# Performance work log

Measured on AMD Instinct MI355X. Metric: run time of the kernel, lower is better.

Reference implementation:

```python
import jax, jax.numpy as jnp
import numpy as np

B, N, E, K = 4, 8192, 1024, 2048  # batch, points, emb_dims, pool nodes (N//4)
KNN = 20


def _conv(w, x):  # 1x1 Conv1d, no bias: w [O,C], x [B,C,N]
    return jnp.einsum('oc,bcn->bon', w, x)


def _bn(x, s, b):  # eval-mode BN folded to per-channel scale/bias, x [B,C,N]
    return x * s[None, :, None] + b[None, :, None]


def _sqdist(a, b):  # a [B,3,N], b [B,3,M] -> [B,N,M] squared distances
    return ((a * a).sum(1)[:, :, None] + (b * b).sum(1)[:, None, :]
            - 2.0 * jnp.einsum('bcn,bcm->bnm', a, b))


def _bgather(f, idx):  # f [B,C,N], idx [B,...] -> [B,C,...]
    return jax.vmap(lambda ff, ii: ff[:, ii])(f, idx)


def _pool(xyz, feat, pw, pb, k):
    Bq, C, _ = feat.shape
    proj = _conv(pw, feat) + pb[None, :, None]          # [B,8C,N]
    vec = proj.max(-1).reshape(Bq, C, 8)                # [B,C,8]
    scores = jax.nn.sigmoid(jnp.einsum('bcn,bce->bne', feat, vec))  # [B,N,8]
    v, i = jax.lax.top_k(scores.transpose(0, 2, 1), k // 8)         # [B,8,k//8]
    values = v.transpose(0, 2, 1).reshape(Bq, -1)       # [B,k] (torch reshape order)
    idx = i.transpose(0, 2, 1).reshape(Bq, -1)
    node_static = _bgather(xyz, idx)                    # [B,3,k]
    node_feature = _bgather(feat, idx) * values[:, None, :]
    node = node_static * values[:, None, :]
    return node, node_feature, node_static


def _aggregate(xyz, node, feat, k):
    d = _sqdist(xyz, node)                               # [B,N,M]
    _, idx = jax.lax.top_k(-d.transpose(0, 2, 1), k)     # [B,M,k] nearest inputs per node
    grouped = _bgather(feat, idx)                        # [B,C,M,k]
    return grouped.max(-1)                               # [B,C,M]


def _unpool(node_xyz, unknown_xyz, feat):
    d = _sqdist(unknown_xyz, node_xyz)                   # [B,N,M]
    negd, idx = jax.lax.top_k(-d, 3)                     # 3-NN along M
    w = jax.nn.softmax(-negd, axis=-1)                   # softmax over sq-dists (faithful)
    grouped = _bgather(feat, idx)                        # [B,C,N,3]
    return (w[:, None, :, :] * grouped).sum(-1)


def _forward(x, conv1_w, bn1_s, bn1_b, conv2_w, bn2_s, bn2_b,
             conv2m_w, bn2m_s, bn2m_b, pool_w, pool_b,
             conv3_w, bn3_s, bn3_b, conv4_w, bn4_s, bn4_b,
             conv5_w, bn5_s, bn5_b, conv6_w, bn6c_s, bn6c_b,
             conv7_w, bn7c_s, bn7c_b, conv8_w, bn8_s, bn8_b,
             conv9_w, bn9_s, bn9_b, conv10_w,
             lin1_w, bn6h_s, bn6h_b, lin2_w, lin2_b, bn7h_s, bn7h_b,
             lin3_w, lin3_b):
    relu = jax.nn.relu
    xyz = x
    x1 = relu(_bn(_conv(conv1_w, x), bn1_s, bn1_b))      # [B,64,N]
    x2 = relu(_bn(_conv(conv2_w, x1), bn2_s, bn2_b))     # [B,64,N]
    xt1_ = jnp.concatenate([x1, x2], 1)                  # [B,128,N]
    xt1 = relu(_bn(_conv(conv2m_w, xt1_), bn2m_s, bn2m_b))  # [B,E,N]
    node1, nf1, node1_static = _pool(xyz, xt1_, pool_w, pool_b, K)
    agg = _aggregate(xyz, node1, xt1_, KNN)              # [B,128,K]
    h = jnp.concatenate([nf1, agg], 1)                   # [B,256,K]
    x3 = relu(_bn(_conv(conv3_w, h), bn3_s, bn3_b))
    x4 = relu(_bn(_conv(conv4_w, x3), bn4_s, bn4_b))
    xt2 = relu(_bn(_conv(conv5_w, jnp.concatenate([x3, x4], 1)), bn5_s, bn5_b))
    vector = jnp.concatenate([xt1.max(-1), xt2.max(-1)], 1)  # [B,2E]
    c = relu((vector @ lin1_w.T) * bn6h_s + bn6h_b)
    c = relu((c @ lin2_w.T + lin2_b) * bn7h_s + bn7h_b)
    logits_cls = c @ lin3_w.T + lin3_b                   # [B,15]
    vrep = jnp.broadcast_to(vector[:, :, None], (vector.shape[0], vector.shape[1], x4.shape[-1]))
    s = relu(_bn(_conv(conv6_w, jnp.concatenate([vrep, x4], 1)), bn6c_s, bn6c_b))
    s = relu(_bn(_conv(conv7_w, jnp.concatenate([s, x3], 1)), bn7c_s, bn7c_b))
    s = _unpool(node1, xyz, s)                           # [B,128,N]
    s = relu(_bn(_conv(conv8_w, jnp.concatenate([s, x2], 1)), bn8_s, bn8_b))
    s = relu(_bn(_conv(conv9_w, jnp.concatenate([s, x1], 1)), bn9_s, bn9_b))
    logits_seg = _conv(conv10_w, s)                      # [B,2,N]
    return (logits_cls, logits_seg, node1, node1_static)


def setup_inputs() -> dict:
    key = jax.random.key(0)
    keys = iter(jax.random.split(key, 80))
    def w(shape, scale=0.05):
        return jax.random.normal(next(keys), shape, jnp.float32) * scale
    inp = {'x': jax.random.normal(next(keys), (B, 3, N), jnp.float32)}
    conv_shapes = {'conv1_w': (64, 3), 'conv2_w': (64, 64), 'conv2m_w': (E, 128),
                   'conv3_w': (256, 256), 'conv4_w': (256, 256), 'conv5_w': (E, 512),
                   'conv6_w': (128, 2 * E + 256), 'conv7_w': (128, 384),
                   'conv8_w': (128, 192), 'conv9_w': (128, 192), 'conv10_w': (2, 128)}
    for n, s in conv_shapes.items():
        inp[n] = w(s)
    for n, c in [('bn1', 64), ('bn2', 64), ('bn2m', E), ('bn3', 256), ('bn4', 256),
                 ('bn5', E), ('bn6c', 128), ('bn7c', 128), ('bn8', 128), ('bn9', 128),
                 ('bn6h', 512), ('bn7h', 256)]:
        inp[n + '_s'] = 1.0 + w((c,))
        inp[n + '_b'] = w((c,))
    inp['pool_w'] = w((E, 128)); inp['pool_b'] = w((E,))
    inp['lin1_w'] = w((512, 2 * E))
    inp['lin2_w'] = w((256, 512)); inp['lin2_b'] = w((256,))
    inp['lin3_w'] = w((15, 256)); inp['lin3_b'] = w((15,))
    return inp


def reference(x, conv1_w, bn1_s, bn1_b, conv2_w, bn2_s, bn2_b,
              conv2m_w, bn2m_s, bn2m_b, pool_w, pool_b,
              conv3_w, bn3_s, bn3_b, conv4_w, bn4_s, bn4_b,
              conv5_w, bn5_s, bn5_b, conv6_w, bn6c_s, bn6c_b,
              conv7_w, bn7c_s, bn7c_b, conv8_w, bn8_s, bn8_b,
              conv9_w, bn9_s, bn9_b, conv10_w,
              lin1_w, bn6h_s, bn6h_b, lin2_w, lin2_b, bn7h_s, bn7h_b,
              lin3_w, lin3_b):
    return _forward(x, conv1_w, bn1_s, bn1_b, conv2_w, bn2_s, bn2_b,
                    conv2m_w, bn2m_s, bn2m_b, pool_w, pool_b,
                    conv3_w, bn3_s, bn3_b, conv4_w, bn4_s, bn4_b,
                    conv5_w, bn5_s, bn5_b, conv6_w, bn6c_s, bn6c_b,
                    conv7_w, bn7c_s, bn7c_b, conv8_w, bn8_s, bn8_b,
                    conv9_w, bn9_s, bn9_b, conv10_w,
                    lin1_w, bn6h_s, bn6h_b, lin2_w, lin2_b, bn7h_s, bn7h_b,
                    lin3_w, lin3_b)
```

## Files before the change

### kernel.cpp

```cpp
#include <hip/hip_runtime.h>
#include <math.h>

#define NPTS 8192
#define MNODE 2048

#define WS_XT1  0L
#define WS_A    4194304L
#define WS_B    8388608L
#define WS_C    12582912L
#define WS_D    14680064L
#define WS_TOPV 18874368L
#define WS_TOPI 18882560L
#define WS_NODE 18890752L
#define WS_MAXP 18915328L
#define WS_VEC  18919424L
#define WS_C1   18927616L
#define WS_C2   18929664L
#define WS_B6   18930688L
#define WS_K20  18931200L
#define WS_K3I  19095040L
#define WS_K3W  19193344L

__global__ __launch_bounds__(256) void k_conv1(const float* __restrict__ x,
                                               const float* __restrict__ W,
                                               const float* __restrict__ sc,
                                               const float* __restrict__ bi,
                                               float* __restrict__ out) {
    int t = blockIdx.x * 256 + threadIdx.x;
    int n = t & 8191, o = (t >> 13) & 63, b = t >> 19;
    const float* xb = x + (long)b * 3 * NPTS;
    float a = W[o * 3 + 0] * xb[n] + W[o * 3 + 1] * xb[NPTS + n] + W[o * 3 + 2] * xb[2 * NPTS + n];
    a = fmaxf(a * sc[o] + bi[o], 0.f);
    out[((long)b * 128 + o) * NPTS + n] = a;
}

__global__ __launch_bounds__(256) void k_conv2(const float* __restrict__ in,
                                               const float* __restrict__ W,
                                               const float* __restrict__ sc,
                                               const float* __restrict__ bi,
                                               float* __restrict__ out) {
    int t = blockIdx.x * 256 + threadIdx.x;
    int n = t & 8191, o = (t >> 13) & 63, b = t >> 19;
    const float* ip = in + (long)b * 128 * NPTS + n;
    const float* wp = W + o * 64;
    float a = 0.f;
#pragma unroll 8
    for (int c = 0; c < 64; ++c) a = fmaf(wp[c], ip[(long)c * NPTS], a);
    out[((long)b * 128 + 64 + o) * NPTS + n] = fmaxf(a * sc[o] + bi[o], 0.f);
}

#define CMAX_FMA16()                                                        \
    {                                                                       \
        const float4* wp4 = reinterpret_cast<const float4*>(Wl + c16);      \
        _Pragma("unroll")                                                   \
        for (int g = 0; g < 4; ++g) {                                       \
            float4 w = wp4[g];                                              \
            acc[4 * g + 0].x = fmaf(w.x, v.x, acc[4 * g + 0].x);            \
            acc[4 * g + 0].y = fmaf(w.x, v.y, acc[4 * g + 0].y);            \
            acc[4 * g + 0].z = fmaf(w.x, v.z, acc[4 * g + 0].z);            \
            acc[4 * g + 0].w = fmaf(w.x, v.w, acc[4 * g + 0].w);            \
            acc[4 * g + 1].x = fmaf(w.y, v.x, acc[4 * g + 1].x);            \
            acc[4 * g + 1].y = fmaf(w.y, v.y, acc[4 * g + 1].y);            \
            acc[4 * g + 1].z = fmaf(w.y, v.z, acc[4 * g + 1].z);            \
            acc[4 * g + 1].w = fmaf(w.y, v.w, acc[4 * g + 1].w);            \
            acc[4 * g + 2].x = fmaf(w.z, v.x, acc[4 * g + 2].x);            \
            acc[4 * g + 2].y = fmaf(w.z, v.y, acc[4 * g + 2].y);            \
            acc[4 * g + 2].z = fmaf(w.z, v.z, acc[4 * g + 2].z);            \
            acc[4 * g + 2].w = fmaf(w.z, v.w, acc[4 * g + 2].w);            \
            acc[4 * g + 3].x = fmaf(w.w, v.x, acc[4 * g + 3].x);            \
            acc[4 * g + 3].y = fmaf(w.w, v.y, acc[4 * g + 3].y);            \
            acc[4 * g + 3].z = fmaf(w.w, v.z, acc[4 * g + 3].z);            \
            acc[4 * g + 3].w = fmaf(w.w, v.w, acc[4 * g + 3].w);            \
        }                                                                   \
    }

__global__ __launch_bounds__(256) void k_convmax(
        const float* __restrict__ in, int C, long ibs,
        const float* __restrict__ W1, const float* __restrict__ cb1,
        const float* __restrict__ sc1, const float* __restrict__ bi1, int relu1,
        float* __restrict__ pmax1,
        const float* __restrict__ W2, const float* __restrict__ cb2,
        const float* __restrict__ sc2, const float* __restrict__ bi2, int relu2,
        float* __restrict__ pmax2,
        int wpitch, int O, int Nn) {
    extern __shared__ float sm_[];
    float* Wl = sm_;
    float* red = sm_ + 16 * C;
    int b = blockIdx.z;
    int ns = blockIdx.x;
    int oblocks = O >> 4;
    int setid = (int)blockIdx.y / oblocks;
    int og0 = ((int)blockIdx.y - setid * oblocks) * 16;
    const float* W  = setid ? W2 : W1;
    const float* cb = setid ? cb2 : cb1;
    const float* sc = setid ? sc2 : sc1;
    const float* bi = setid ? bi2 : bi1;
    int do_relu     = setid ? relu2 : relu1;
    float* pmax     = setid ? pmax2 : pmax1;
    for (int t = threadIdx.x; t < 16 * C; t += 256) {
        int c = t >> 4, o = t & 15;
        Wl[t] = W[(long)(og0 + o) * wpitch + c];
    }
    __syncthreads();
    int n0 = ns * 1024 + threadIdx.x * 4;
    float4 acc[16];
#pragma unroll
    for (int o = 0; o < 16; ++o) acc[o] = make_float4(0.f, 0.f, 0.f, 0.f);
    const float* p = in + (long)b * ibs + n0;
    float4 v = *reinterpret_cast<const float4*>(p);
    for (int c = 0; c < C - 1; ++c) {
        float4 vn = *reinterpret_cast<const float4*>(p + (long)(c + 1) * Nn);
        int c16 = c * 16;
        CMAX_FMA16();
        v = vn;
    }
    {
        int c16 = (C - 1) * 16;
        CMAX_FMA16();
    }
#pragma unroll
    for (int o = 0; o < 16; ++o) {
        float cbv = cb ? cb[og0 + o] : 0.f;
        float scv = sc ? sc[og0 + o] : 1.f;
        float biv = bi ? bi[og0 + o] : 0.f;
        float4 a = acc[o];
        float vx = (a.x + cbv) * scv + biv;
        float vy = (a.y + cbv) * scv + biv;
        float vz = (a.z + cbv) * scv + biv;
        float vw = (a.w + cbv) * scv + biv;
        if (do_relu) {
            vx = fmaxf(vx, 0.f); vy = fmaxf(vy, 0.f);
            vz = fmaxf(vz, 0.f); vw = fmaxf(vw, 0.f);
        }
        red[o * 257 + threadIdx.x] = fmaxf(fmaxf(vx, vy), fmaxf(vz, vw));
    }
    __syncthreads();
    for (int ls = 7; ls >= 0; --ls) {
        int s = 1 << ls;
        for (int w = threadIdx.x; w < 16 * s; w += 256) {
            int o = w >> ls, i = w & (s - 1);
            float* r = red + o * 257;
            r[i] = fmaxf(r[i], r[i + s]);
        }
        __syncthreads();
    }
    if (threadIdx.x < 16)
        pmax[((long)ns * 4 + b) * O + og0 + threadIdx.x] = red[threadIdx.x * 257];
}

__global__ __launch_bounds__(256) void k_maxred(const float* __restrict__ pmax, int nsplit,
                                                int O, float* __restrict__ out, long obs) {
    int t = blockIdx.x * 256 + threadIdx.x;
    if (t >= 4 * O) return;
    int o = t % O, b = t / O;
    float m = -3.0e38f;
    for (int s = 0; s < nsplit; ++s) m = fmaxf(m, pmax[((long)s * 4 + b) * O + o]);
    out[(long)b * obs + o] = m;
}

#define CONV_FMA8()                                                         \
    {                                                                       \
        const float4* wp4 = reinterpret_cast<const float4*>(Wl + c8);       \
        _Pragma("unroll")                                                   \
        for (int g = 0; g < 2; ++g) {                                       \
            float4 w = wp4[g];                                              \
            acc[4 * g + 0].x = fmaf(w.x, v.x, acc[4 * g + 0].x);            \
            acc[4 * g + 0].y = fmaf(w.x, v.y, acc[4 * g + 0].y);            \
            acc[4 * g + 0].z = fmaf(w.x, v.z, acc[4 * g + 0].z);            \
            acc[4 * g + 0].w = fmaf(w.x, v.w, acc[4 * g + 0].w);            \
            acc[4 * g + 1].x = fmaf(w.y, v.x, acc[4 * g + 1].x);            \
            acc[4 * g + 1].y = fmaf(w.y, v.y, acc[4 * g + 1].y);            \
            acc[4 * g + 1].z = fmaf(w.y, v.z, acc[4 * g + 1].z);            \
            acc[4 * g + 1].w = fmaf(w.y, v.w, acc[4 * g + 1].w);            \
            acc[4 * g + 2].x = fmaf(w.z, v.x, acc[4 * g + 2].x);            \
            acc[4 * g + 2].y = fmaf(w.z, v.y, acc[4 * g + 2].y);            \
            acc[4 * g + 2].z = fmaf(w.z, v.z, acc[4 * g + 2].z);            \
            acc[4 * g + 2].w = fmaf(w.z, v.w, acc[4 * g + 2].w);            \
            acc[4 * g + 3].x = fmaf(w.w, v.x, acc[4 * g + 3].x);            \
            acc[4 * g + 3].y = fmaf(w.w, v.y, acc[4 * g + 3].y);            \
            acc[4 * g + 3].z = fmaf(w.w, v.z, acc[4 * g + 3].z);            \
            acc[4 * g + 3].w = fmaf(w.w, v.w, acc[4 * g + 3].w);            \
        }                                                                   \
    }

__global__ __launch_bounds__(256) void k_conv(const float* __restrict__ in1, int C1, long ibs1,
                                              const float* __restrict__ in2, int C2, long ibs2,
                                              const float* __restrict__ W, int wpitch,
                                              const float* __restrict__ extra,
                                              const float* __restrict__ sc,
                                              const float* __restrict__ bi, int do_relu,
                                              float* __restrict__ out, long obs, int O, int Nn) {
    __shared__ float Wl[384 * 8];
    int b = blockIdx.z;
    int og0 = blockIdx.y * 8;
    int on = O - og0; if (on > 8) on = 8;
    int Ct = C1 + C2;
    for (int t = threadIdx.x; t < Ct * 8; t += 256) {
        int c = t >> 3, o = t & 7;
        Wl[t] = (o < on) ? W[(long)(og0 + o) * wpitch + c] : 0.f;
    }
    __syncthreads();
    int n0 = blockIdx.x * 1024 + threadIdx.x * 4;
    float4 acc[8];
#pragma unroll
    for (int o = 0; o < 8; ++o) acc[o] = make_float4(0.f, 0.f, 0.f, 0.f);
    const float* p1 = in1 + (long)b * ibs1 + n0;
    {
        float4 v = *reinterpret_cast<const float4*>(p1);
        for (int c = 0; c < C1 - 1; ++c) {
            float4 vn = *reinterpret_cast<const float4*>(p1 + (long)(c + 1) * Nn);
            int c8 = c * 8;
            CONV_FMA8();
            v = vn;
        }
        int c8 = (C1 - 1) * 8;
        CONV_FMA8();
    }
    if (in2) {
        const float* p2 = in2 + (long)b * ibs2 + n0;
        float4 v = *reinterpret_cast<const float4*>(p2);
        for (int c = 0; c < C2 - 1; ++c) {
            float4 vn = *reinterpret_cast<const float4*>(p2 + (long)(c + 1) * Nn);
            int c8 = (C1 + c) * 8;
            CONV_FMA8();
            v = vn;
        }
        int c8 = (Ct - 1) * 8;
        CONV_FMA8();
    }
#pragma unroll
    for (int o = 0; o < 8; ++o) {
        if (o < on) {
            float e = extra ? extra[(long)b * O + og0 + o] : 0.f;
            float s = sc ? sc[og0 + o] : 1.f;
            float bv = bi ? bi[og0 + o] : 0.f;
            float4 a = acc[o];
            a.x = (a.x + e) * s + bv;
            a.y = (a.y + e) * s + bv;
            a.z = (a.z + e) * s + bv;
            a.w = (a.w + e) * s + bv;
            if (do_relu) {
                a.x = fmaxf(a.x, 0.f); a.y = fmaxf(a.y, 0.f);
                a.z = fmaxf(a.z, 0.f); a.w = fmaxf(a.w, 0.f);
            }
            *reinterpret_cast<float4*>(out + (long)b * obs + (long)(og0 + o) * Nn + n0) = a;
        }
    }
}

__global__ __launch_bounds__(256) void k_scores(const float* __restrict__ feat,
                                                const float* __restrict__ maxp,
                                                float* __restrict__ scores) {
    __shared__ float vl[1024];
    int b = blockIdx.z;
    for (int t = threadIdx.x; t < 1024; t += 256) vl[t] = maxp[b * 1024 + t];
    __syncthreads();
    int n0 = blockIdx.x * 1024 + threadIdx.x * 4;
    float4 acc[8];
#pragma unroll
    for (int e = 0; e < 8; ++e) acc[e] = make_float4(0.f, 0.f, 0.f, 0.f);
    const float* p = feat + (long)b * 128 * NPTS + n0;
    for (int c = 0; c < 128; ++c) {
        float4 v = *reinterpret_cast<const float4*>(p + (long)c * NPTS);
#pragma unroll
        for (int e = 0; e < 8; ++e) {
            float w = vl[c * 8 + e];
            acc[e].x = fmaf(w, v.x, acc[e].x);
            acc[e].y = fmaf(w, v.y, acc[e].y);
            acc[e].z = fmaf(w, v.z, acc[e].z);
            acc[e].w = fmaf(w, v.w, acc[e].w);
        }
    }
#pragma unroll
    for (int e = 0; e < 8; ++e) {
        float4 a = acc[e];
        a.x = 1.f / (1.f + expf(-a.x));
        a.y = 1.f / (1.f + expf(-a.y));
        a.z = 1.f / (1.f + expf(-a.z));
        a.w = 1.f / (1.f + expf(-a.w));
        *reinterpret_cast<float4*>(scores + ((long)b * 8 + e) * NPTS + n0) = a;
    }
}

__global__ __launch_bounds__(256) void k_sorta(const float* __restrict__ scores,
                                               unsigned int* __restrict__ kout,
                                               unsigned short* __restrict__ iout) {
    __shared__ unsigned int kv[1024];
    __shared__ unsigned short ki[1024];
    int ch = blockIdx.x & 7;
    const float* sp = scores + (long)(blockIdx.x >> 3) * NPTS + ch * 1024;
    for (int t = threadIdx.x; t < 1024; t += 256) {
        kv[t] = __float_as_uint(sp[t]) ^ 0xFFFFFFFFu;
        ki[t] = (unsigned short)(ch * 1024 + t);
    }
    __syncthreads();
    for (int k = 2; k <= 1024; k <<= 1) {
        for (int j = k >> 1; j > 0; j >>= 1) {
            for (int t = threadIdx.x; t < 1024; t += 256) {
                int ixj = t ^ j;
                if (ixj > t) {
                    unsigned int va = kv[t], vb = kv[ixj];
                    unsigned short ia = ki[t], ib = ki[ixj];
                    bool up = ((t & k) == 0);
                    bool gt = (va > vb) || (va == vb && ia > ib);
                    if (gt == up) { kv[t] = vb; kv[ixj] = va; ki[t] = ib; ki[ixj] = ia; }
                }
            }
            __syncthreads();
        }
    }
    if (threadIdx.x < 256) {
        kout[blockIdx.x * 256 + threadIdx.x] = kv[threadIdx.x];
        iout[blockIdx.x * 256 + threadIdx.x] = ki[threadIdx.x];
    }
}

__global__ __launch_bounds__(512) void k_sortb(const unsigned int* __restrict__ kin,
                                               const unsigned short* __restrict__ iin,
                                               float* __restrict__ topv,
                                               int* __restrict__ topi) {
    __shared__ unsigned int kv[2048];
    __shared__ unsigned short ki[2048];
    int be = blockIdx.x, b = be >> 3, e = be & 7;
    for (int t = threadIdx.x; t < 2048; t += 512) {
        kv[t] = kin[be * 2048 + t];
        ki[t] = iin[be * 2048 + t];
    }
    __syncthreads();
    for (int k = 2; k <= 2048; k <<= 1) {
        for (int j = k >> 1; j > 0; j >>= 1) {
            for (int t = threadIdx.x; t < 2048; t += 512) {
                int ixj = t ^ j;
                if (ixj > t) {
                    unsigned int va = kv[t], vb = kv[ixj];
                    unsigned short ia = ki[t], ib = ki[ixj];
                    bool up = ((t & k) == 0);
                    bool gt = (va > vb) || (va == vb && ia > ib);
                    if (gt == up) { kv[t] = vb; kv[ixj] = va; ki[t] = ib; ki[ixj] = ia; }
                }
            }
            __syncthreads();
        }
    }
    for (int r = threadIdx.x; r < 256; r += 512) {
        int j = r * 8 + e;
        topv[b * 2048 + j] = __uint_as_float(kv[r] ^ 0xFFFFFFFFu);
        topi[b * 2048 + j] = (int)ki[r];
    }
}

__global__ __launch_bounds__(256) void k_poolgather(const float* __restrict__ xyz,
                                                    const float* __restrict__ topv,
                                                    const int* __restrict__ topi,
                                                    float* __restrict__ node_ws,
                                                    float* __restrict__ out_node,
                                                    float* __restrict__ out_nstat) {
    int t = blockIdx.x * 256 + threadIdx.x;
    int j = t & 2047, b = t >> 11;
    int i = topi[b * 2048 + j];
    float v = topv[b * 2048 + j];
#pragma unroll
    for (int k = 0; k < 3; ++k) {
        float sx = xyz[((long)b * 3 + k) * NPTS + i];
        float nd = sx * v;
        out_nstat[((long)b * 3 + k) * MNODE + j] = sx;
        out_node[((long)b * 3 + k) * MNODE + j] = nd;
        node_ws[((long)b * 3 + k) * MNODE + j] = nd;
    }
}

__global__ __launch_bounds__(256) void k_nf1(const float* __restrict__ feat,
                                             const float* __restrict__ topv,
                                             const int* __restrict__ topi,
                                             float* __restrict__ h) {
    int t = blockIdx.x * 256 + threadIdx.x;
    int j = t & 2047, c = (t >> 11) & 127, b = t >> 18;
    int i = topi[b * 2048 + j];
    float v = topv[b * 2048 + j];
    h[((long)b * 256 + c) * MNODE + j] = feat[((long)b * 128 + c) * NPTS + i] * v;
}

__device__ __forceinline__ unsigned int fsortbits(float f) {
    unsigned int u = __float_as_uint(f);
    return u ^ ((unsigned int)((int)u >> 31) | 0x80000000u);
}

__global__ __launch_bounds__(256) void k_knn20(const float* __restrict__ xyz,
                                               const float* __restrict__ node,
                                               int* __restrict__ k20) {
    __shared__ unsigned int s1[256];
    __shared__ int s2[256];
    __shared__ int lcnt;
    int m = blockIdx.x & 2047, b = blockIdx.x >> 11;
    int t = threadIdx.x;
    float nx = node[((long)b * 3 + 0) * MNODE + m];
    float ny = node[((long)b * 3 + 1) * MNODE + m];
    float nz = node[((long)b * 3 + 2) * MNODE + m];
    float sm = nx * nx + ny * ny + nz * nz;
    const float* xb = xyz + (long)b * 3 * NPTS;
    unsigned int kmin = 0xFFFFFFFFu;
    for (int i = 0; i < 32; ++i) {
        int n = i * 256 + t;
        float px = xb[n], py = xb[NPTS + n], pz = xb[2 * NPTS + n];
        float d = (px * px + py * py + pz * pz) + sm - 2.f * (px * nx + py * ny + pz * nz);
        unsigned int key = fsortbits(d);
        kmin = key < kmin ? key : kmin;
    }
    s1[t] = kmin;
    if (t == 0) lcnt = 0;
    __syncthreads();
    for (int k = 2; k <= 256; k <<= 1) {
        for (int j = k >> 1; j > 0; j >>= 1) {
            int ixj = t ^ j;
            if (ixj > t) {
                unsigned int va = s1[t], vb = s1[ixj];
                bool up = ((t & k) == 0);
                if ((va > vb) == up) { s1[t] = vb; s1[ixj] = va; }
            }
            __syncthreads();
        }
    }
    unsigned int keyT = s1[19];
    __syncthreads();
    for (int i = 0; i < 32; ++i) {
        int n = i * 256 + t;
        float px = xb[n], py = xb[NPTS + n], pz = xb[2 * NPTS + n];
        float d = (px * px + py * py + pz * pz) + sm - 2.f * (px * nx + py * ny + pz * nz);
        unsigned int key = fsortbits(d);
        if (key <= keyT) {
            int p = atomicAdd(&lcnt, 1);
            if (p < 128) { s1[p] = key; s2[p] = n; }
        }
    }
    __syncthreads();
    int cnt = lcnt;
    if (cnt <= 128) {
        if (t >= cnt && t < 128) { s1[t] = 0xFFFFFFFFu; s2[t] = 0x7FFFFFFF; }
        __syncthreads();
        for (int k = 2; k <= 128; k <<= 1) {
            for (int j = k >> 1; j > 0; j >>= 1) {
                if (t < 128) {
                    int ixj = t ^ j;
                    if (ixj > t) {
                        unsigned int va = s1[t], vb = s1[ixj];
                        int ia = s2[t], ib = s2[ixj];
                        bool up = ((t & k) == 0);
                        bool gt = (va > vb) || (va == vb && ia > ib);
                        if (gt == up) { s1[t] = vb; s1[ixj] = va; s2[t] = ib; s2[ixj] = ia; }
                    }
                }
                __syncthreads();
            }
        }
        if (t < 20) k20[((long)b * 2048 + m) * 20 + t] = s2[t];
    } else {
        unsigned int lastk = 0u; int lasti = -1;
        for (int r = 0; r < 20; ++r) {
            unsigned int bk = 0xFFFFFFFFu; int bi = 0x7FFFFFFF;
            for (int i = 0; i < 32; ++i) {
                int n = i * 256 + t;
                float px = xb[n], py = xb[NPTS + n], pz = xb[2 * NPTS + n];
                float d = (px * px + py * py + pz * pz) + sm - 2.f * (px * nx + py * ny + pz * nz);
                unsigned int key = fsortbits(d);
                bool gtlast = (key > lastk) || (key == lastk && n > lasti);
                bool ltbest = (key < bk) || (key == bk && n < bi);
                if (gtlast && ltbest) { bk = key; bi = n; }
            }
            s1[t] = bk; s2[t] = bi;
            __syncthreads();
            for (int s = 128; s > 0; s >>= 1) {
                if (t < s) {
                    unsigned int vo = s1[t + s]; int io = s2[t + s];
                    unsigned int vm = s1[t]; int im = s2[t];
                    if (vo < vm || (vo == vm && io < im)) { s1[t] = vo; s2[t] = io; }
                }
                __syncthreads();
            }
            if (t == 0) k20[((long)b * 2048 + m) * 20 + r] = s2[0];
            lastk = s1[0]; lasti = s2[0];
            __syncthreads();
        }
    }
}

__global__ __launch_bounds__(256) void k_agg(const float* __restrict__ feat,
                                             const int* __restrict__ k20,
                                             float* __restrict__ h) {
    int t = blockIdx.x * 256 + threadIdx.x;
    int m = t & 2047, c = (t >> 11) & 127, b = t >> 18;
    const int* ip = k20 + ((long)b * 2048 + m) * 20;
    const float* fb = feat + ((long)b * 128 + c) * NPTS;
    float mx = -3.0e38f;
#pragma unroll
    for (int q = 0; q < 20; ++q) mx = fmaxf(mx, fb[ip[q] & 8191]);
    h[((long)b * 256 + 128 + c) * MNODE + m] = mx;
}

__global__ __launch_bounds__(256) void k_gemv(const float* __restrict__ in, int C,
                                              const float* __restrict__ W, int wpitch,
                                              const float* __restrict__ lb,
                                              const float* __restrict__ sc,
                                              const float* __restrict__ bi, int do_relu,
                                              float* __restrict__ out, int O) {
    __shared__ float red[256];
    int o = blockIdx.x;
    int t = threadIdx.x;
    const float* wp = W + (long)o * wpitch;
    float a0 = 0.f, a1 = 0.f, a2 = 0.f, a3 = 0.f;
    for (int c = t * 4; c < C; c += 1024) {
        float4 w = *reinterpret_cast<const float4*>(wp + c);
        float4 v0 = *reinterpret_cast<const float4*>(in + 0L * C + c);
        float4 v1 = *reinterpret_cast<const float4*>(in + 1L * C + c);
        float4 v2 = *reinterpret_cast<const float4*>(in + 2L * C + c);
        float4 v3 = *reinterpret_cast<const float4*>(in + 3L * C + c);
        a0 += w.x * v0.x + w.y * v0.y + w.z * v0.z + w.w * v0.w;
        a1 += w.x * v1.x + w.y * v1.y + w.z * v1.z + w.w * v1.w;
        a2 += w.x * v2.x + w.y * v2.y + w.z * v2.z + w.w * v2.w;
        a3 += w.x * v3.x + w.y * v3.y + w.z * v3.z + w.w * v3.w;
    }
    float lbv = lb ? lb[o] : 0.f;
    float scv = sc ? sc[o] : 1.f;
    float biv = bi ? bi[o] : 0.f;
#pragma unroll
    for (int b = 0; b < 4; ++b) {
        float a = (b == 0) ? a0 : (b == 1) ? a1 : (b == 2) ? a2 : a3;
        __syncthreads();
        red[t] = a;
        __syncthreads();
        for (int s2 = 128; s2 > 0; s2 >>= 1) {
            if (t < s2) red[t] += red[t + s2];
            __syncthreads();
        }
        if (t == 0) {
            float r = (red[0] + lbv) * scv + biv;
            if (do_relu) r = fmaxf(r, 0.f);
            out[(long)b * O + o] = r;
        }
    }
}

__global__ __launch_bounds__(256) void k_knn3(const float* __restrict__ xyz,
                                              const float* __restrict__ node,
                                              int* __restrict__ k3i, float* __restrict__ k3w) {
    __shared__ float sx[2048], sy[2048], sz[2048], sn[2048];
    __shared__ float md[256][3];
    __shared__ int   mi[256][3];
    int b = blockIdx.x >> 8;
    int pbase = (blockIdx.x & 255) * 32;
    int t = threadIdx.x;
    const float* nb = node + (long)b * 3 * MNODE;
    for (int j = t; j < 2048; j += 256) {
        float qx = nb[j], qy = nb[MNODE + j], qz = nb[2 * MNODE + j];
        sx[j] = qx; sy[j] = qy; sz[j] = qz;
        sn[j] = qx * qx + qy * qy + qz * qz;
    }
    __syncthreads();
    int i = t & 31, q = t >> 5;
    int n = pbase + i;
    float px = xyz[((long)b * 3 + 0) * NPTS + n];
    float py = xyz[((long)b * 3 + 1) * NPTS + n];
    float pz = xyz[((long)b * 3 + 2) * NPTS + n];
    float sp = px * px + py * py + pz * pz;
    float d0 = 3.0e38f, d1 = 3.0e38f, d2 = 3.0e38f;
    int i0 = 0, i1 = 0, i2 = 0;
    int m0 = q * 256;
#pragma unroll 4
    for (int k = 0; k < 256; ++k) {
        int m = m0 + k;
        float d = (sp + sn[m]) - 2.f * (px * sx[m] + py * sy[m] + pz * sz[m]);
        if (d < d2) {
            d2 = d; i2 = m;
            if (d2 < d1) { float td = d1; d1 = d2; d2 = td; int ti = i1; i1 = i2; i2 = ti; }
            if (d1 < d0) { float td = d0; d0 = d1; d1 = td; int ti = i0; i0 = i1; i1 = ti; }
        }
    }
    md[t][0] = d0; md[t][1] = d1; md[t][2] = d2;
    mi[t][0] = i0; mi[t][1] = i1; mi[t][2] = i2;
    __syncthreads();
    if (t < 32) {
        int p0 = 0, p1 = 0, p2 = 0, p3 = 0, p4 = 0, p5 = 0, p6 = 0, p7 = 0;
        float rd[3]; int ri[3];
#pragma unroll
        for (int r = 0; r < 3; ++r) {
            float bestd = 3.0e38f; int besti = 0x7FFFFFFF; int bestq = -1;
#define KNN3_HEAD(QQ, PV)                                                              \
            {                                                                          \
                float dd = md[(QQ) * 32 + t][PV]; int ii = mi[(QQ) * 32 + t][PV];      \
                if (dd < bestd || (dd == bestd && ii < besti)) {                       \
                    bestd = dd; besti = ii; bestq = (QQ);                              \
                }                                                                      \
            }
            KNN3_HEAD(0, p0) KNN3_HEAD(1, p1) KNN3_HEAD(2, p2) KNN3_HEAD(3, p3)
            KNN3_HEAD(4, p4) KNN3_HEAD(5, p5) KNN3_HEAD(6, p6) KNN3_HEAD(7, p7)
#undef KNN3_HEAD
            rd[r] = bestd; ri[r] = besti;
            p0 += (bestq == 0); p1 += (bestq == 1); p2 += (bestq == 2); p3 += (bestq == 3);
            p4 += (bestq == 4); p5 += (bestq == 5); p6 += (bestq == 6); p7 += (bestq == 7);
        }
        float mxd = fmaxf(rd[0], fmaxf(rd[1], rd[2]));
        float e0 = expf(rd[0] - mxd), e1 = expf(rd[1] - mxd), e2 = expf(rd[2] - mxd);
        float inv = 1.f / (e0 + e1 + e2);
        long base = ((long)b * NPTS + pbase + t) * 3;
        k3i[base] = ri[0]; k3i[base + 1] = ri[1]; k3i[base + 2] = ri[2];
        k3w[base] = e0 * inv; k3w[base + 1] = e1 * inv; k3w[base + 2] = e2 * inv;
    }
}

__global__ __launch_bounds__(256) void k_unpool(const float* __restrict__ s7,
                                                const int* __restrict__ k3i,
                                                const float* __restrict__ k3w,
                                                float* __restrict__ sup) {
    int t = blockIdx.x * 256 + threadIdx.x;
    int n = t & 8191, c = (t >> 13) & 127, b = t >> 20;
    long base = ((long)b * NPTS + n) * 3;
    const float* spp = s7 + ((long)b * 128 + c) * MNODE;
    float a = k3w[base] * spp[k3i[base]] + k3w[base + 1] * spp[k3i[base + 1]] +
              k3w[base + 2] * spp[k3i[base + 2]];
    sup[((long)b * 128 + c) * NPTS + n] = a;
}

extern "C" void kernel_launch(void* const* d_in, const int* in_sizes, int n_in,
                              void* d_out, int out_size, void* d_ws, size_t ws_size,
                              hipStream_t stream) {
    const float* x     = (const float*)d_in[0];
    const float* c1w   = (const float*)d_in[1];
    const float* c2w   = (const float*)d_in[2];
    const float* c2mw  = (const float*)d_in[3];
    const float* c3w   = (const float*)d_in[4];
    const float* c4w   = (const float*)d_in[5];
    const float* c5w   = (const float*)d_in[6];
    const float* c6w   = (const float*)d_in[7];
    const float* c7w   = (const float*)d_in[8];
    const float* c8w   = (const float*)d_in[9];
    const float* c9w   = (const float*)d_in[10];
    const float* c10w  = (const float*)d_in[11];
    const float* bn1s  = (const float*)d_in[12]; const float* bn1b  = (const float*)d_in[13];
    const float* bn2s  = (const float*)d_in[14]; const float* bn2b  = (const float*)d_in[15];
    const float* bn2ms = (const float*)d_in[16]; const float* bn2mb = (const float*)d_in[17];
    const float* bn3s  = (const float*)d_in[18]; const float* bn3b  = (const float*)d_in[19];
    const float* bn4s  = (const float*)d_in[20]; const float* bn4b  = (const float*)d_in[21];
    const float* bn5s  = (const float*)d_in[22]; const float* bn5b  = (const float*)d_in[23];
    const float* bn6cs = (const float*)d_in[24]; const float* bn6cb = (const float*)d_in[25];
    const float* bn7cs = (const float*)d_in[26]; const float* bn7cb = (const float*)d_in[27];
    const float* bn8s  = (const float*)d_in[28]; const float* bn8b  = (const float*)d_in[29];
    const float* bn9s  = (const float*)d_in[30]; const float* bn9b  = (const float*)d_in[31];
    const float* bn6hs = (const float*)d_in[32]; const float* bn6hb = (const float*)d_in[33];
    const float* bn7hs = (const float*)d_in[34]; const float* bn7hb = (const float*)d_in[35];
    const float* poolw = (const float*)d_in[36]; const float* poolb = (const float*)d_in[37];
    const float* l1w   = (const float*)d_in[38];
    const float* l2w   = (const float*)d_in[39]; const float* l2b   = (const float*)d_in[40];
    const float* l3w   = (const float*)d_in[41]; const float* l3b   = (const float*)d_in[42];

    float* ws   = (float*)d_ws;
    float* xt1  = ws + WS_XT1;
    float* x34  = ws + WS_A;
    float* scor = ws + WS_B;
    float* s8   = ws + WS_B;
    float* hbuf = ws + WS_C;
    float* s6   = ws + WS_C;
    float* s7   = ws + WS_C + 1048576L;
    float* sup  = ws + WS_D;
    float* s9   = ws + WS_D;
    float* topv = ws + WS_TOPV;
    int*   topi = (int*)(ws + WS_TOPI);
    float* node = ws + WS_NODE;
    float* maxp = ws + WS_MAXP;
    float* vec  = ws + WS_VEC;
    float* c1b  = ws + WS_C1;
    float* c2b_ = ws + WS_C2;
    float* b6   = ws + WS_B6;
    int*   k20  = (int*)(ws + WS_K20);
    float* pmax1 = ws + WS_K20;
    float* pmax2 = ws + WS_K20 + 32768;
    int*   k3i  = (int*)(ws + WS_K3I);
    float* k3w  = ws + WS_K3W;
    unsigned int*   sskeys = (unsigned int*)(ws + WS_A);
    unsigned short* ssidx  = (unsigned short*)(ws + WS_A + 65536);

    float* out       = (float*)d_out;
    float* out_cls   = out;
    float* out_seg   = out + 60;
    float* out_node  = out + 60 + 65536;
    float* out_nstat = out_node + 24576;

    k_conv1<<<dim3(8192), dim3(256), 0, stream>>>(x, c1w, bn1s, bn1b, xt1);
    k_conv2<<<dim3(8192), dim3(256), 0, stream>>>(xt1, c2w, bn2s, bn2b, xt1);
    k_convmax<<<dim3(8, 128, 4), dim3(256), (16 * 128 + 16 * 257) * 4, stream>>>(
        xt1, 128, 128L * NPTS,
        c2mw, nullptr, bn2ms, bn2mb, 1, pmax1,
        poolw, poolb, nullptr, nullptr, 0, pmax2,
        128, 1024, NPTS);
    k_maxred<<<dim3(16), dim3(256), 0, stream>>>(pmax1, 8, 1024, vec, 2048);
    k_maxred<<<dim3(16), dim3(256), 0, stream>>>(pmax2, 8, 1024, maxp, 1024);
    k_scores<<<dim3(8, 1, 4), dim3(256), 0, stream>>>(xt1, maxp, scor);
    k_sorta<<<dim3(256), dim3(256), 0, stream>>>(scor, sskeys, ssidx);
    k_sortb<<<dim3(32), dim3(512), 0, stream>>>(sskeys, ssidx, topv, topi);
    k_poolgather<<<dim3(32), dim3(256), 0, stream>>>(x, topv, topi, node, out_node, out_nstat);
    k_nf1<<<dim3(4096), dim3(256), 0, stream>>>(xt1, topv, topi, hbuf);
    k_knn20<<<dim3(8192), dim3(256), 0, stream>>>(x, node, k20);
    k_agg<<<dim3(4096), dim3(256), 0, stream>>>(xt1, k20, hbuf);
    k_conv<<<dim3(2, 32, 4), dim3(256), 0, stream>>>(hbuf, 256, 256L * MNODE, nullptr, 0, 0,
                                                     c3w, 256, nullptr, bn3s, bn3b, 1,
                                                     x34, 512L * MNODE, 256, MNODE);
    k_conv<<<dim3(2, 32, 4), dim3(256), 0, stream>>>(x34, 256, 512L * MNODE, nullptr, 0, 0,
                                                     c4w, 256, nullptr, bn4s, bn4b, 1,
                                                     x34 + 256L * MNODE, 512L * MNODE, 256, MNODE);
    k_convmax<<<dim3(2, 64, 4), dim3(256), (16 * 512 + 16 * 257) * 4, stream>>>(
        x34, 512, 512L * MNODE,
        c5w, nullptr, bn5s, bn5b, 1, pmax1,
        nullptr, nullptr, nullptr, nullptr, 0, nullptr,
        512, 1024, MNODE);
    k_maxred<<<dim3(16), dim3(256), 0, stream>>>(pmax1, 2, 1024, vec + 1024, 2048);
    k_gemv<<<dim3(512), dim3(256), 0, stream>>>(vec, 2048, l1w, 2048, nullptr, bn6hs, bn6hb, 1, c1b, 512);
    k_gemv<<<dim3(256), dim3(256), 0, stream>>>(c1b, 512, l2w, 512, l2b, bn7hs, bn7hb, 1, c2b_, 256);
    k_gemv<<<dim3(15), dim3(256), 0, stream>>>(c2b_, 256, l3w, 256, l3b, nullptr, nullptr, 0, out_cls, 15);
    k_gemv<<<dim3(128), dim3(256), 0, stream>>>(vec, 2048, c6w, 2304, nullptr, nullptr, nullptr, 0, b6, 128);
    k_conv<<<dim3(2, 16, 4), dim3(256), 0, stream>>>(x34 + 256L * MNODE, 256, 512L * MNODE,
                                                     nullptr, 0, 0, c6w + 2048, 2304, b6,
                                                     bn6cs, bn6cb, 1, s6, 128L * MNODE, 128, MNODE);
    k_conv<<<dim3(2, 16, 4), dim3(256), 0, stream>>>(s6, 128, 128L * MNODE, x34, 256, 512L * MNODE,
                                                     c7w, 384, nullptr, bn7cs, bn7cb, 1,
                                                     s7, 128L * MNODE, 128, MNODE);
    k_knn3<<<dim3(1024), dim3(256), 0, stream>>>(x, node, k3i, k3w);
    k_unpool<<<dim3(16384), dim3(256), 0, stream>>>(s7, k3i, k3w, sup);
    k_conv<<<dim3(8, 16, 4), dim3(256), 0, stream>>>(sup, 128, 128L * NPTS, xt1 + 64L * NPTS, 64,
                                                     128L * NPTS, c8w, 192, nullptr, bn8s, bn8b, 1,
                                                     s8, 128L * NPTS, 128, NPTS);
    k_conv<<<dim3(8, 16, 4), dim3(256), 0, stream>>>(s8, 128, 128L * NPTS, xt1, 64, 128L * NPTS,
                                                     c9w, 192, nullptr, bn9s, bn9b, 1,
                                                     s9, 128L * NPTS, 128, NPTS);
    k_conv<<<dim3(8, 1, 4), dim3(256), 0, stream>>>(s9, 128, 128L * NPTS, nullptr, 0, 0,
                                                    c10w, 128, nullptr, nullptr, nullptr, 0,
                                                    out_seg, 2L * NPTS, 2, NPTS);
    (void)in_sizes; (void)n_in; (void)out_size; (void)ws_size;
}
```

Before: 1.004 ms.

## Widen conv output tile to 16, split score kernel per expert, double-buffer convmax loads

k_conv now computes 16 output channels per block instead of 8 using the shared FMA16 macro, so each input load is reused twice as often and grids halve in y. k_scores is split across 8 blocks along y, one per score channel, reducing per-thread accumulators and adding parallelism at the cost of reading the features 8 times. k_convmax loads two channels ahead per iteration to deepen prefetch. The wider tile raises register pressure and lowers block count, which may hurt occupancy. The final conv with O=2 now wastes more of its 16-wide tile.

```diff
diff --git a/kernel.cpp b/kernel.cpp
--- a/kernel.cpp
+++ b/kernel.cpp
@@ -107,17 +107,18 @@
 #pragma unroll
     for (int o = 0; o < 16; ++o) acc[o] = make_float4(0.f, 0.f, 0.f, 0.f);
     const float* p = in + (long)b * ibs + n0;
-    float4 v = *reinterpret_cast<const float4*>(p);
-    for (int c = 0; c < C - 1; ++c) {
-        float4 vn = *reinterpret_cast<const float4*>(p + (long)(c + 1) * Nn);
-        int c16 = c * 16;
-        CMAX_FMA16();
-        v = vn;
-    }
-    {
-        int c16 = (C - 1) * 16;
-        CMAX_FMA16();
-    }
+    float4 v0 = *reinterpret_cast<const float4*>(p);
+    float4 v1 = *reinterpret_cast<const float4*>(p + Nn);
+    int c = 0;
+    for (; c + 2 < C; c += 2) {
+        float4 n2 = *reinterpret_cast<const float4*>(p + (long)(c + 2) * Nn);
+        float4 n3 = *reinterpret_cast<const float4*>(p + (long)(c + 3) * Nn);
+        { int c16 = c * 16; float4 v = v0; CMAX_FMA16(); }
+        { int c16 = (c + 1) * 16; float4 v = v1; CMAX_FMA16(); }
+        v0 = n2; v1 = n3;
+    }
+    { int c16 = (C - 2) * 16; float4 v = v0; CMAX_FMA16(); }
+    { int c16 = (C - 1) * 16; float4 v = v1; CMAX_FMA16(); }
 #pragma unroll
     for (int o = 0; o < 16; ++o) {
         float cbv = cb ? cb[og0 + o] : 0.f;
@@ -158,31 +159,6 @@
     out[(long)b * obs + o] = m;
 }
 
-#define CONV_FMA8()                                                         \
-    {                                                                       \
-        const float4* wp4 = reinterpret_cast<const float4*>(Wl + c8);       \
-        _Pragma("unroll")                                                   \
-        for (int g = 0; g < 2; ++g) {                                       \
-            float4 w = wp4[g];                                              \
-            acc[4 * g + 0].x = fmaf(w.x, v.x, acc[4 * g + 0].x);            \
-            acc[4 * g + 0].y = fmaf(w.x, v.y, acc[4 * g + 0].y);            \
-            acc[4 * g + 0].z = fmaf(w.x, v.z, acc[4 * g + 0].z);            \
-            acc[4 * g + 0].w = fmaf(w.x, v.w, acc[4 * g + 0].w);            \
-            acc[4 * g + 1].x = fmaf(w.y, v.x, acc[4 * g + 1].x);            \
-            acc[4 * g + 1].y = fmaf(w.y, v.y, acc[4 * g + 1].y);            \
-            acc[4 * g + 1].z = fmaf(w.y, v.z, acc[4 * g + 1].z);            \
-            acc[4 * g + 1].w = fmaf(w.y, v.w, acc[4 * g + 1].w);            \
-            acc[4 * g + 2].x = fmaf(w.z, v.x, acc[4 * g + 2].x);            \
-            acc[4 * g + 2].y = fmaf(w.z, v.y, acc[4 * g + 2].y);            \
-            acc[4 * g + 2].z = fmaf(w.z, v.z, acc[4 * g + 2].z);            \
-            acc[4 * g + 2].w = fmaf(w.z, v.w, acc[4 * g + 2].w);            \
-            acc[4 * g + 3].x = fmaf(w.w, v.x, acc[4 * g + 3].x);            \
-            acc[4 * g + 3].y = fmaf(w.w, v.y, acc[4 * g + 3].y);            \
-            acc[4 * g + 3].z = fmaf(w.w, v.z, acc[4 * g + 3].z);            \
-            acc[4 * g + 3].w = fmaf(w.w, v.w, acc[4 * g + 3].w);            \
-        }                                                                   \
-    }
-
 __global__ __launch_bounds__(256) void k_conv(const float* __restrict__ in1, int C1, long ibs1,
                                               const float* __restrict__ in2, int C2, long ibs2,
                                               const float* __restrict__ W, int wpitch,
@@ -190,46 +166,46 @@
                                               const float* __restrict__ sc,
                                               const float* __restrict__ bi, int do_relu,
                                               float* __restrict__ out, long obs, int O, int Nn) {
-    __shared__ float Wl[384 * 8];
+    __shared__ float Wl[384 * 16];
     int b = blockIdx.z;
-    int og0 = blockIdx.y * 8;
-    int on = O - og0; if (on > 8) on = 8;
+    int og0 = blockIdx.y * 16;
+    int on = O - og0; if (on > 16) on = 16;
     int Ct = C1 + C2;
-    for (int t = threadIdx.x; t < Ct * 8; t += 256) {
-        int c = t >> 3, o = t & 7;
+    for (int t = threadIdx.x; t < Ct * 16; t += 256) {
+        int c = t >> 4, o = t & 15;
         Wl[t] = (o < on) ? W[(long)(og0 + o) * wpitch + c] : 0.f;
     }
     __syncthreads();
     int n0 = blockIdx.x * 1024 + threadIdx.x * 4;
-    float4 acc[8];
+    float4 acc[16];
 #pragma unroll
-    for (int o = 0; o < 8; ++o) acc[o] = make_float4(0.f, 0.f, 0.f, 0.f);
+    for (int o = 0; o < 16; ++o) acc[o] = make_float4(0.f, 0.f, 0.f, 0.f);
     const float* p1 = in1 + (long)b * ibs1 + n0;
     {
         float4 v = *reinterpret_cast<const float4*>(p1);
         for (int c = 0; c < C1 - 1; ++c) {
             float4 vn = *reinterpret_cast<const float4*>(p1 + (long)(c + 1) * Nn);
-            int c8 = c * 8;
-            CONV_FMA8();
+            int c16 = c * 16;
+            CMAX_FMA16();
             v = vn;
         }
-        int c8 = (C1 - 1) * 8;
-        CONV_FMA8();
+        int c16 = (C1 - 1) * 16;
+        CMAX_FMA16();
     }
     if (in2) {
         const float* p2 = in2 + (long)b * ibs2 + n0;
         float4 v = *reinterpret_cast<const float4*>(p2);
         for (int c = 0; c < C2 - 1; ++c) {
             float4 vn = *reinterpret_cast<const float4*>(p2 + (long)(c + 1) * Nn);
-            int c8 = (C1 + c) * 8;
-            CONV_FMA8();
+            int c16 = (C1 + c) * 16;
+            CMAX_FMA16();
             v = vn;
         }
-        int c8 = (Ct - 1) * 8;
-        CONV_FMA8();
+        int c16 = (Ct - 1) * 16;
+        CMAX_FMA16();
     }
 #pragma unroll
-    for (int o = 0; o < 8; ++o) {
+    for (int o = 0; o < 16; ++o) {
         if (o < on) {
             float e = extra ? extra[(long)b * O + og0 + o] : 0.f;
             float s = sc ? sc[og0 + o] : 1.f;
@@ -251,35 +227,35 @@
 __global__ __launch_bounds__(256) void k_scores(const float* __restrict__ feat,
                                                 const float* __restrict__ maxp,
                                                 float* __restrict__ scores) {
-    __shared__ float vl[1024];
-    int b = blockIdx.z;
-    for (int t = threadIdx.x; t < 1024; t += 256) vl[t] = maxp[b * 1024 + t];
+    __shared__ float wl[128];
+    int b = blockIdx.z, e = blockIdx.y;
+    if (threadIdx.x < 128) wl[threadIdx.x] = maxp[b * 1024 + threadIdx.x * 8 + e];
     __syncthreads();
     int n0 = blockIdx.x * 1024 + threadIdx.x * 4;
-    float4 acc[8];
-#pragma unroll
-    for (int e = 0; e < 8; ++e) acc[e] = make_float4(0.f, 0.f, 0.f, 0.f);
+    float4 acc = make_float4(0.f, 0.f, 0.f, 0.f);
     const float* p = feat + (long)b * 128 * NPTS + n0;
-    for (int c = 0; c < 128; ++c) {
-        float4 v = *reinterpret_cast<const float4*>(p + (long)c * NPTS);
-#pragma unroll
-        for (int e = 0; e < 8; ++e) {
-            float w = vl[c * 8 + e];
-            acc[e].x = fmaf(w, v.x, acc[e].x);
-            acc[e].y = fmaf(w, v.y, acc[e].y);
-            acc[e].z = fmaf(w, v.z, acc[e].z);
-            acc[e].w = fmaf(w, v.w, acc[e].w);
-        }
-    }
-#pragma unroll
-    for (int e = 0; e < 8; ++e) {
-        float4 a = acc[e];
-        a.x = 1.f / (1.f + expf(-a.x));
-        a.y = 1.f / (1.f + expf(-a.y));
-        a.z = 1.f / (1.f + expf(-a.z));
-        a.w = 1.f / (1.f + expf(-a.w));
-        *reinterpret_cast<float4*>(scores + ((long)b * 8 + e) * NPTS + n0) = a;
-    }
+    float4 v = *reinterpret_cast<const float4*>(p);
+    for (int c = 0; c < 127; ++c) {
+        float4 vn = *reinterpret_cast<const float4*>(p + (long)(c + 1) * NPTS);
+        float w = wl[c];
+        acc.x = fmaf(w, v.x, acc.x);
+        acc.y = fmaf(w, v.y, acc.y);
+        acc.z = fmaf(w, v.z, acc.z);
+        acc.w = fmaf(w, v.w, acc.w);
+        v = vn;
+    }
+    {
+        float w = wl[127];
+        acc.x = fmaf(w, v.x, acc.x);
+        acc.y = fmaf(w, v.y, acc.y);
+        acc.z = fmaf(w, v.z, acc.z);
+        acc.w = fmaf(w, v.w, acc.w);
+    }
+    acc.x = 1.f / (1.f + expf(-acc.x));
+    acc.y = 1.f / (1.f + expf(-acc.y));
+    acc.z = 1.f / (1.f + expf(-acc.z));
+    acc.w = 1.f / (1.f + expf(-acc.w));
+    *reinterpret_cast<float4*>(scores + ((long)b * 8 + e) * NPTS + n0) = acc;
 }
 
 __global__ __launch_bounds__(256) void k_sorta(const float* __restrict__ scores,
@@ -692,17 +668,17 @@
         128, 1024, NPTS);
     k_maxred<<<dim3(16), dim3(256), 0, stream>>>(pmax1, 8, 1024, vec, 2048);
     k_maxred<<<dim3(16), dim3(256), 0, stream>>>(pmax2, 8, 1024, maxp, 1024);
-    k_scores<<<dim3(8, 1, 4), dim3(256), 0, stream>>>(xt1, maxp, scor);
+    k_scores<<<dim3(8, 8, 4), dim3(256), 0, stream>>>(xt1, maxp, scor);
     k_sorta<<<dim3(256), dim3(256), 0, stream>>>(scor, sskeys, ssidx);
     k_sortb<<<dim3(32), dim3(512), 0, stream>>>(sskeys, ssidx, topv, topi);
     k_poolgather<<<dim3(32), dim3(256), 0, stream>>>(x, topv, topi, node, out_node, out_nstat);
     k_nf1<<<dim3(4096), dim3(256), 0, stream>>>(xt1, topv, topi, hbuf);
     k_knn20<<<dim3(8192), dim3(256), 0, stream>>>(x, node, k20);
     k_agg<<<dim3(4096), dim3(256), 0, stream>>>(xt1, k20, hbuf);
-    k_conv<<<dim3(2, 32, 4), dim3(256), 0, stream>>>(hbuf, 256, 256L * MNODE, nullptr, 0, 0,
+    k_conv<<<dim3(2, 16, 4), dim3(256), 0, stream>>>(hbuf, 256, 256L * MNODE, nullptr, 0, 0,
                                                      c3w, 256, nullptr, bn3s, bn3b, 1,
                                                      x34, 512L * MNODE, 256, MNODE);
-    k_conv<<<dim3(2, 32, 4), dim3(256), 0, stream>>>(x34, 256, 512L * MNODE, nullptr, 0, 0,
+    k_conv<<<dim3(2, 16, 4), dim3(256), 0, stream>>>(x34, 256, 512L * MNODE, nullptr, 0, 0,
                                                      c4w, 256, nullptr, bn4s, bn4b, 1,
                                                      x34 + 256L * MNODE, 512L * MNODE, 256, MNODE);
     k_convmax<<<dim3(2, 64, 4), dim3(256), (16 * 512 + 16 * 257) * 4, stream>>>(
@@ -715,20 +691,20 @@
     k_gemv<<<dim3(256), dim3(256), 0, stream>>>(c1b, 512, l2w, 512, l2b, bn7hs, bn7hb, 1, c2b_, 256);
     k_gemv<<<dim3(15), dim3(256), 0, stream>>>(c2b_, 256, l3w, 256, l3b, nullptr, nullptr, 0, out_cls, 15);
     k_gemv<<<dim3(128), dim3(256), 0, stream>>>(vec, 2048, c6w, 2304, nullptr, nullptr, nullptr, 0, b6, 128);
-    k_conv<<<dim3(2, 16, 4), dim3(256), 0, stream>>>(x34 + 256L * MNODE, 256, 512L * MNODE,
-                                                     nullptr, 0, 0, c6w + 2048, 2304, b6,
-                                                     bn6cs, bn6cb, 1, s6, 128L * MNODE, 128, MNODE);
-    k_conv<<<dim3(2, 16, 4), dim3(256), 0, stream>>>(s6, 128, 128L * MNODE, x34, 256, 512L * MNODE,
-                                                     c7w, 384, nullptr, bn7cs, bn7cb, 1,
-                                                     s7, 128L * MNODE, 128, MNODE);
+    k_conv<<<dim3(2, 8, 4), dim3(256), 0, stream>>>(x34 + 256L * MNODE, 256, 512L * MNODE,
+                                                    nullptr, 0, 0, c6w + 2048, 2304, b6,
+                                                    bn6cs, bn6cb, 1, s6, 128L * MNODE, 128, MNODE);
+    k_conv<<<dim3(2, 8, 4), dim3(256), 0, stream>>>(s6, 128, 128L * MNODE, x34, 256, 512L * MNODE,
+                                                    c7w, 384, nullptr, bn7cs, bn7cb, 1,
+                                                    s7, 128L * MNODE, 128, MNODE);
     k_knn3<<<dim3(1024), dim3(256), 0, stream>>>(x, node, k3i, k3w);
     k_unpool<<<dim3(16384), dim3(256), 0, stream>>>(s7, k3i, k3w, sup);
-    k_conv<<<dim3(8, 16, 4), dim3(256), 0, stream>>>(sup, 128, 128L * NPTS, xt1 + 64L * NPTS, 64,
-                                                     128L * NPTS, c8w, 192, nullptr, bn8s, bn8b, 1,
-                                                     s8, 128L * NPTS, 128, NPTS);
-    k_conv<<<dim3(8, 16, 4), dim3(256), 0, stream>>>(s8, 128, 128L * NPTS, xt1, 64, 128L * NPTS,
-                                                     c9w, 192, nullptr, bn9s, bn9b, 1,
-                                                     s9, 128L * NPTS, 128, NPTS);
+    k_conv<<<dim3(8, 8, 4), dim3(256), 0, stream>>>(sup, 128, 128L * NPTS, xt1 + 64L * NPTS, 64,
+                                                    128L * NPTS, c8w, 192, nullptr, bn8s, bn8b, 1,
+                                                    s8, 128L * NPTS, 128, NPTS);
+    k_conv<<<dim3(8, 8, 4), dim3(256), 0, stream>>>(s8, 128, 128L * NPTS, xt1, 64, 128L * NPTS,
+                                                    c9w, 192, nullptr, bn9s, bn9b, 1,
+                                                    s9, 128L * NPTS, 128, NPTS);
     k_conv<<<dim3(8, 1, 4), dim3(256), 0, stream>>>(s9, 128, 128L * NPTS, nullptr, 0, 0,
                                                     c10w, 128, nullptr, nullptr, nullptr, 0,
                                                     out_seg, 2L * NPTS, 2, NPTS);
```

Result: slower. 1.040 ms (+3.5%).
